# Performance work log

Measured on AMD Instinct MI355X. Metric: run time of the kernel, lower is better.

## Reference

```python
import jax, jax.numpy as jnp
import numpy as np

EPS = 0.1
N_ITERS = 50


def setup_inputs() -> dict:
    key = jax.random.key(0)
    ks = jax.random.split(key, 4)
    B, C, D, H, W = 2, 64, 4, 16, 32
    feat1 = jax.random.normal(ks[0], (B, C, D, H, W), jnp.float32)
    feat2 = jax.random.normal(ks[1], (B, C, D, H, W), jnp.float32)
    w1 = jax.random.normal(ks[2], (C, 2 * C), jnp.float32) * 0.05  # Conv3d(2C->C, k=1)
    b1 = jnp.zeros((C,), jnp.float32)
    w2 = jax.random.normal(ks[3], (C, C), jnp.float32) * 0.05      # Conv3d(C->C, k=1)
    b2 = jnp.zeros((C,), jnp.float32)
    return {"feat1": feat1, "feat2": feat2, "w1": w1, "b1": b1, "w2": w2, "b2": b2}


def reference(feat1, feat2, w1, b1, w2, b2):
    B, C = feat1.shape[0], feat1.shape[1]
    M = int(np.prod(feat1.shape[2:]))
    seq1 = feat1.reshape(B, C, M).transpose(0, 2, 1)  # [B,M,C]
    seq2 = feat2.reshape(B, C, M).transpose(0, 2, 1)  # [B,M,C]
    # squared euclidean distance = cdist(.,p=2)**2
    sq1 = jnp.sum(seq1 * seq1, axis=-1)               # [B,M]
    sq2 = jnp.sum(seq2 * seq2, axis=-1)               # [B,M]
    cross = jnp.einsum('bmc,bnc->bmn', seq1, seq2)    # [B,M,M]
    C_mat = jnp.maximum(sq1[:, :, None] + sq2[:, None, :] - 2.0 * cross, 0.0)
    log_K = -C_mat / EPS

    def step(lk, _):
        lk = lk - jax.nn.logsumexp(lk, axis=2, keepdims=True)  # row normalize
        lk = lk - jax.nn.logsumexp(lk, axis=1, keepdims=True)  # col normalize
        return lk, None

    log_K, _ = jax.lax.scan(jax.checkpoint(step), log_K, None, length=N_ITERS)
    P = jnp.exp(log_K)                                # [B,M,M]
    fused_ot = jnp.einsum('bmn,bnc->bcm', P, seq2)    # [B,C,M]

    # adaptive gating fusion: two 1x1x1 convs == channel matmuls
    f1 = feat1.reshape(B, C, M)
    cat = jnp.concatenate([f1, fused_ot], axis=1)     # [B,2C,M]
    h = jax.nn.relu(jnp.einsum('oc,bcm->bom', w1, cat) + b1[None, :, None])
    gate = jax.nn.sigmoid(jnp.einsum('oc,bcm->bom', w2, h) + b2[None, :, None])
    fused = gate * f1 + (1.0 - gate) * fused_ot
    return fused.reshape(feat1.shape)
```

## Files before the change

kernel.cpp:

```cpp
#include <hip/hip_runtime.h>
#include <hip/hip_bf16.h>

#define MM 2048
#define CC 64
#define NEG_EPS_INV (-10.0f)

__global__ __launch_bounds__(256) void k_tr(const float* __restrict__ f2,
                                            float* __restrict__ s2t) {
    __shared__ float t[64 * 65];
    int bx = blockIdx.x;
    int b = bx >> 5, nc = bx & 31;
    int tid = threadIdx.x;
    int col = tid & 63, cp = tid >> 6;
    const size_t fbase = (size_t)b * CC * MM;
    for (int it = 0; it < 16; ++it) {
        int c = it * 4 + cp;
        t[c * 65 + col] = f2[fbase + (size_t)c * MM + nc * 64 + col];
    }
    __syncthreads();
    int w = tid >> 6, lane = tid & 63;
    for (int i = 0; i < 16; ++i) {
        int nn = w * 16 + i;
        s2t[((size_t)b * MM + nc * 64 + nn) * 64 + lane] = t[lane * 65 + nn];
    }
}

__global__ __launch_bounds__(256) void k_build(const float* __restrict__ f1,
                                               const float* __restrict__ f2,
                                               float* __restrict__ K0,
                                               float* __restrict__ K0T, int useT) {
    __shared__ float f1s[64 * 64];
    __shared__ float f2s[64 * 64];
    __shared__ float kt[64 * 65];
    __shared__ float sq1s[64], sq2s[64];
    int bx = blockIdx.x;
    int b = bx >> 10, mt = (bx >> 5) & 31, nt = bx & 31;
    int tid = threadIdx.x;
    int w = tid >> 6, lane = tid & 63;
    int col = tid & 63, cp = tid >> 6;
    const size_t fbase = (size_t)b * CC * MM;
    for (int it = 0; it < 16; ++it) {
        int c = it * 4 + cp;
        f1s[c * 64 + col] = f1[fbase + (size_t)c * MM + mt * 64 + col];
        f2s[c * 64 + col] = f2[fbase + (size_t)c * MM + nt * 64 + col];
    }
    __syncthreads();
    if (tid < 64) {
        float s = 0.f;
        for (int c = 0; c < 64; ++c) { float x = f1s[c * 64 + tid]; s = fmaf(x, x, s); }
        sq1s[tid] = s;
    } else if (tid < 128) {
        int n = tid - 64;
        float s = 0.f;
        for (int c = 0; c < 64; ++c) { float x = f2s[c * 64 + n]; s = fmaf(x, x, s); }
        sq2s[n] = s;
    }
    __syncthreads();
    float acc[16];
#pragma unroll
    for (int i = 0; i < 16; ++i) acc[i] = 0.f;
    for (int c = 0; c < 64; ++c) {
        float f2v = f2s[c * 64 + lane];
#pragma unroll
        for (int i = 0; i < 16; ++i)
            acc[i] = fmaf(f1s[c * 64 + w * 16 + i], f2v, acc[i]);
    }
    float sq2v = sq2s[lane];
    size_t kbase = ((size_t)b * MM + mt * 64 + w * 16) * MM + nt * 64 + lane;
#pragma unroll
    for (int i = 0; i < 16; ++i) {
        float r = sq1s[w * 16 + i] + sq2v - 2.f * acc[i];
        r = fmaxf(r, 0.f);
        float kv = NEG_EPS_INV * r;
        K0[kbase + (size_t)i * MM] = kv;
        kt[(w * 16 + i) * 65 + lane] = kv;
    }
    if (useT) {
        __syncthreads();
        size_t tbase = ((size_t)b * MM + nt * 64 + w * 16) * MM + mt * 64 + lane;
#pragma unroll
        for (int i = 0; i < 16; ++i)
            K0T[tbase + (size_t)i * MM] = kt[lane * 65 + (w * 16 + i)];
    }
}

__global__ __launch_bounds__(256) void k_lse(const float* __restrict__ K,
                                             const float* __restrict__ vin,
                                             float* __restrict__ uout) {
    int bx = blockIdx.x;
    int b = bx >> 9, rg = bx & 511;
    int w = threadIdx.x >> 6, lane = threadIdx.x & 63;
    int m = rg * 4 + w;
    const float* rowp = K + ((size_t)b * MM + m) * MM;
    const float* vp = vin + (size_t)b * MM;
    float x[32];
#pragma unroll
    for (int j = 0; j < 8; ++j) {
        float4 kv = *(const float4*)(rowp + j * 256 + lane * 4);
        float4 vv = *(const float4*)(vp + j * 256 + lane * 4);
        x[j * 4 + 0] = kv.x + vv.x;
        x[j * 4 + 1] = kv.y + vv.y;
        x[j * 4 + 2] = kv.z + vv.z;
        x[j * 4 + 3] = kv.w + vv.w;
    }
    float mx = x[0];
#pragma unroll
    for (int i = 1; i < 32; ++i) mx = fmaxf(mx, x[i]);
#pragma unroll
    for (int off = 32; off >= 1; off >>= 1) mx = fmaxf(mx, __shfl_xor(mx, off));
    float s = 0.f;
#pragma unroll
    for (int i = 0; i < 32; ++i) s += __expf(x[i] - mx);
#pragma unroll
    for (int off = 32; off >= 1; off >>= 1) s += __shfl_xor(s, off);
    if (lane == 0) uout[(size_t)b * MM + m] = -(mx + __logf(s));
}

__global__ __launch_bounds__(1024) void k_colfb(const float* __restrict__ K,
                                                const float* __restrict__ uin,
                                                float* __restrict__ vout) {
    __shared__ float pm[16 * 64], ps[16 * 64];
    int bx = blockIdx.x;
    int b = bx >> 5, nc = bx & 31;
    int w = threadIdx.x >> 6, lane = threadIdx.x & 63;
    int n = nc * 64 + lane;
    const float* up = uin + (size_t)b * MM;
    float mx = -3.0e38f, s = 0.f;
    size_t base = ((size_t)b * MM + w * 128) * MM + n;
    for (int mm = 0; mm < 128; ++mm) {
        float x = K[base + (size_t)mm * MM] + up[w * 128 + mm];
        float nm = fmaxf(mx, x);
        s = s * __expf(mx - nm) + __expf(x - nm);
        mx = nm;
    }
    pm[w * 64 + lane] = mx;
    ps[w * 64 + lane] = s;
    __syncthreads();
    if (w == 0) {
        float M2 = pm[lane];
        for (int i = 1; i < 16; ++i) M2 = fmaxf(M2, pm[i * 64 + lane]);
        float S = 0.f;
        for (int i = 0; i < 16; ++i) S += ps[i * 64 + lane] * __expf(pm[i * 64 + lane] - M2);
        vout[(size_t)b * MM + n] = -(M2 + __logf(S));
    }
}

__global__ __launch_bounds__(256) void k_fot(const float* __restrict__ K0,
                                             const float* __restrict__ u,
                                             const float* __restrict__ v,
                                             const float* __restrict__ s2t,
                                             float* __restrict__ fot) {
    extern __shared__ float plds[];
    int bx = blockIdx.x;
    int b = bx >> 8, mg = (bx >> 2) & 63, ns = bx & 3;
    int w = threadIdx.x >> 6, lane = threadIdx.x & 63;
    int m0 = mg * 32 + w * 8;
    float* pw = plds + w * 512 * 8;
    const float* vp = v + (size_t)b * MM + ns * 512;
#pragma unroll
    for (int r = 0; r < 8; ++r) {
        const float* krow = K0 + ((size_t)b * MM + m0 + r) * MM + ns * 512;
        float uv = u[(size_t)b * MM + m0 + r];
        for (int j = 0; j < 8; ++j) {
            int nn = j * 64 + lane;
            pw[nn * 8 + r] = __expf(krow[nn] + uv + vp[nn]);
        }
    }
    __syncthreads();
    float acc[8];
#pragma unroll
    for (int r = 0; r < 8; ++r) acc[r] = 0.f;
    const float* s2p = s2t + ((size_t)b * MM + ns * 512) * 64 + lane;
    for (int nn = 0; nn < 512; ++nn) {
        float s2 = s2p[(size_t)nn * 64];
        float4 p0 = *(const float4*)(pw + nn * 8);
        float4 p1 = *(const float4*)(pw + nn * 8 + 4);
        acc[0] = fmaf(p0.x, s2, acc[0]);
        acc[1] = fmaf(p0.y, s2, acc[1]);
        acc[2] = fmaf(p0.z, s2, acc[2]);
        acc[3] = fmaf(p0.w, s2, acc[3]);
        acc[4] = fmaf(p1.x, s2, acc[4]);
        acc[5] = fmaf(p1.y, s2, acc[5]);
        acc[6] = fmaf(p1.z, s2, acc[6]);
        acc[7] = fmaf(p1.w, s2, acc[7]);
    }
#pragma unroll
    for (int r = 0; r < 8; ++r)
        atomicAdd(&fot[((size_t)b * MM + m0 + r) * 64 + lane], acc[r]);
}

__global__ __launch_bounds__(256) void k_gate(const float* __restrict__ f1,
                                              const float* __restrict__ fot,
                                              const float* __restrict__ w1,
                                              const float* __restrict__ b1,
                                              const float* __restrict__ w2,
                                              const float* __restrict__ b2,
                                              float* __restrict__ out) {
    __shared__ float w1s[64 * 129];
    __shared__ float w2s[64 * 65];
    __shared__ float cats[4 * 128];
    __shared__ float hs[4 * 64];
    __shared__ float outs[64 * 5];
    int bx = blockIdx.x;
    int b = bx >> 9, mg = bx & 511;
    int tid = threadIdx.x;
    int w = tid >> 6, lane = tid & 63;
    int m = mg * 4 + w;
    for (int t = 0; t < 32; ++t) {
        int idx = t * 256 + tid;
        w1s[(idx >> 7) * 129 + (idx & 127)] = w1[idx];
    }
    for (int t = 0; t < 16; ++t) {
        int idx = t * 256 + tid;
        w2s[(idx >> 6) * 65 + (idx & 63)] = w2[idx];
    }
    float f1v = f1[(size_t)b * CC * MM + (size_t)lane * MM + m];
    float fov = fot[((size_t)b * MM + m) * 64 + lane];
    cats[w * 128 + lane] = f1v;
    cats[w * 128 + 64 + lane] = fov;
    __syncthreads();
    float hacc = b1[lane];
    for (int c = 0; c < 128; ++c)
        hacc = fmaf(w1s[lane * 129 + c], cats[w * 128 + c], hacc);
    hs[w * 64 + lane] = fmaxf(hacc, 0.f);
    __syncthreads();
    float g = b2[lane];
    for (int c = 0; c < 64; ++c)
        g = fmaf(w2s[lane * 65 + c], hs[w * 64 + c], g);
    g = 1.f / (1.f + __expf(-g));
    float fused = g * f1v + (1.f - g) * fov;
    outs[lane * 5 + w] = fused;
    __syncthreads();
    int o = tid >> 2, mi = tid & 3;
    out[(size_t)b * CC * MM + (size_t)o * MM + mg * 4 + mi] = outs[o * 5 + mi];
}

extern "C" void kernel_launch(void* const* d_in, const int* in_sizes, int n_in,
                              void* d_out, int out_size, void* d_ws, size_t ws_size,
                              hipStream_t stream) {
    const float* feat1 = (const float*)d_in[0];
    const float* feat2 = (const float*)d_in[1];
    const float* w1 = (const float*)d_in[2];
    const float* b1 = (const float*)d_in[3];
    const float* w2 = (const float*)d_in[4];
    const float* b2 = (const float*)d_in[5];
    float* out = (float*)d_out;
    char* ws = (char*)d_ws;

    const size_t S = (size_t)2 * MM * MM * 4;
    const size_t tail = 16384 + 16384 + 1048576 + 1048576;
    int useT = (ws_size >= 2 * S + tail) ? 1 : 0;

    float* K0 = (float*)ws;
    float* K0T = (float*)(ws + S);
    float* tailp = (float*)(ws + (useT ? 2 * S : S));
    float* u = tailp;
    float* v = tailp + 4096;
    float* s2t = v + 4096;
    float* fot = s2t + 262144;

    k_tr<<<64, 256, 0, stream>>>(feat2, s2t);
    k_build<<<2048, 256, 0, stream>>>(feat1, feat2, K0, K0T, useT);
    hipMemsetAsync(v, 0, 16384, stream);
    hipMemsetAsync(fot, 0, 1048576, stream);

    for (int it = 0; it < 50; ++it) {
        k_lse<<<1024, 256, 0, stream>>>(K0, v, u);
        if (useT)
            k_lse<<<1024, 256, 0, stream>>>(K0T, u, v);
        else
            k_colfb<<<64, 1024, 0, stream>>>(K0, u, v);
    }

    k_fot<<<512, 256, 65536, stream>>>(K0, u, v, s2t, fot);
    k_gate<<<1024, 256, 0, stream>>>(feat1, fot, w1, b1, w2, b2, out);
}
```

Before: 833.8 us.

## Fuse Sinkhorn iterations into one persistent kernel with register-resident cost rows

Replaces the 100 separate row/column logsumexp launches with a single persistent kernel of 256 blocks. Each thread keeps its slice of two K rows and two K-transpose rows in registers for all 50 iterations, so the 32 MB cost matrix is not re-read from memory on every pass. Blocks synchronise between half-steps through an atomic-counter grid barrier. The barrier assumes all 256 blocks are co-resident, the wait loop has a timeout guard that could silently break correctness, and the K0T workspace is now always required with no fallback path.

```diff
diff --git a/kernel.cpp b/kernel.cpp
--- a/kernel.cpp
+++ b/kernel.cpp
@@ -4,6 +4,7 @@
 #define MM 2048
 #define CC 64
 #define NEG_EPS_INV (-10.0f)
+#define NBLK 256
 
 __global__ __launch_bounds__(256) void k_tr(const float* __restrict__ f2,
                                             float* __restrict__ s2t) {
@@ -28,7 +29,7 @@
 __global__ __launch_bounds__(256) void k_build(const float* __restrict__ f1,
                                                const float* __restrict__ f2,
                                                float* __restrict__ K0,
-                                               float* __restrict__ K0T, int useT) {
+                                               float* __restrict__ K0T) {
     __shared__ float f1s[64 * 64];
     __shared__ float f2s[64 * 64];
     __shared__ float kt[64 * 65];
@@ -70,78 +71,100 @@
 #pragma unroll
     for (int i = 0; i < 16; ++i) {
         float r = sq1s[w * 16 + i] + sq2v - 2.f * acc[i];
-        r = fmaxf(r, 0.f);
-        float kv = NEG_EPS_INV * r;
+        float kv = NEG_EPS_INV * fmaxf(r, 0.f);
         K0[kbase + (size_t)i * MM] = kv;
         kt[(w * 16 + i) * 65 + lane] = kv;
     }
-    if (useT) {
-        __syncthreads();
-        size_t tbase = ((size_t)b * MM + nt * 64 + w * 16) * MM + mt * 64 + lane;
-#pragma unroll
-        for (int i = 0; i < 16; ++i)
-            K0T[tbase + (size_t)i * MM] = kt[lane * 65 + (w * 16 + i)];
-    }
-}
-
-__global__ __launch_bounds__(256) void k_lse(const float* __restrict__ K,
-                                             const float* __restrict__ vin,
-                                             float* __restrict__ uout) {
-    int bx = blockIdx.x;
-    int b = bx >> 9, rg = bx & 511;
-    int w = threadIdx.x >> 6, lane = threadIdx.x & 63;
-    int m = rg * 4 + w;
-    const float* rowp = K + ((size_t)b * MM + m) * MM;
-    const float* vp = vin + (size_t)b * MM;
-    float x[32];
-#pragma unroll
-    for (int j = 0; j < 8; ++j) {
-        float4 kv = *(const float4*)(rowp + j * 256 + lane * 4);
-        float4 vv = *(const float4*)(vp + j * 256 + lane * 4);
-        x[j * 4 + 0] = kv.x + vv.x;
-        x[j * 4 + 1] = kv.y + vv.y;
-        x[j * 4 + 2] = kv.z + vv.z;
-        x[j * 4 + 3] = kv.w + vv.w;
-    }
-    float mx = x[0];
-#pragma unroll
-    for (int i = 1; i < 32; ++i) mx = fmaxf(mx, x[i]);
-#pragma unroll
-    for (int off = 32; off >= 1; off >>= 1) mx = fmaxf(mx, __shfl_xor(mx, off));
-    float s = 0.f;
-#pragma unroll
-    for (int i = 0; i < 32; ++i) s += __expf(x[i] - mx);
-#pragma unroll
-    for (int off = 32; off >= 1; off >>= 1) s += __shfl_xor(s, off);
-    if (lane == 0) uout[(size_t)b * MM + m] = -(mx + __logf(s));
-}
-
-__global__ __launch_bounds__(1024) void k_colfb(const float* __restrict__ K,
-                                                const float* __restrict__ uin,
-                                                float* __restrict__ vout) {
-    __shared__ float pm[16 * 64], ps[16 * 64];
-    int bx = blockIdx.x;
-    int b = bx >> 5, nc = bx & 31;
-    int w = threadIdx.x >> 6, lane = threadIdx.x & 63;
-    int n = nc * 64 + lane;
-    const float* up = uin + (size_t)b * MM;
-    float mx = -3.0e38f, s = 0.f;
-    size_t base = ((size_t)b * MM + w * 128) * MM + n;
-    for (int mm = 0; mm < 128; ++mm) {
-        float x = K[base + (size_t)mm * MM] + up[w * 128 + mm];
-        float nm = fmaxf(mx, x);
-        s = s * __expf(mx - nm) + __expf(x - nm);
-        mx = nm;
-    }
-    pm[w * 64 + lane] = mx;
-    ps[w * 64 + lane] = s;
-    __syncthreads();
-    if (w == 0) {
-        float M2 = pm[lane];
-        for (int i = 1; i < 16; ++i) M2 = fmaxf(M2, pm[i * 64 + lane]);
-        float S = 0.f;
-        for (int i = 0; i < 16; ++i) S += ps[i * 64 + lane] * __expf(pm[i * 64 + lane] - M2);
-        vout[(size_t)b * MM + n] = -(M2 + __logf(S));
+    __syncthreads();
+    size_t tbase = ((size_t)b * MM + nt * 64 + w * 16) * MM + mt * 64 + lane;
+#pragma unroll
+    for (int i = 0; i < 16; ++i)
+        K0T[tbase + (size_t)i * MM] = kt[lane * 65 + (w * 16 + i)];
+}
+
+__device__ __forceinline__ void gbar(int* bar, int slot, int tid) {
+    __syncthreads();
+    if (tid == 0) {
+        __threadfence();
+        atomicAdd(&bar[slot], 1);
+        long guard = 0;
+        while (__hip_atomic_load(&bar[slot], __ATOMIC_RELAXED,
+                                 __HIP_MEMORY_SCOPE_AGENT) < NBLK &&
+               ++guard < (1L << 25)) {
+            __builtin_amdgcn_s_sleep(2);
+        }
+        __threadfence();
+    }
+    __syncthreads();
+}
+
+#define LSE2(KA, KB, SRCP, DSTP)                                         \
+    {                                                                    \
+        float xl[32];                                                    \
+        _Pragma("unroll")                                                \
+        for (int j = 0; j < 8; ++j) {                                    \
+            float4 t = ((const float4*)(SRCP))[j * 64 + lane];           \
+            xl[4*j+0] = t.x; xl[4*j+1] = t.y;                            \
+            xl[4*j+2] = t.z; xl[4*j+3] = t.w;                            \
+        }                                                                \
+        _Pragma("unroll")                                                \
+        for (int r = 0; r < 2; ++r) {                                    \
+            float mx = -3.0e38f;                                         \
+            _Pragma("unroll")                                            \
+            for (int i = 0; i < 32; ++i)                                 \
+                mx = fmaxf(mx, (r == 0 ? KA[i] : KB[i]) + xl[i]);        \
+            _Pragma("unroll")                                            \
+            for (int off = 32; off >= 1; off >>= 1)                      \
+                mx = fmaxf(mx, __shfl_xor(mx, off));                     \
+            float s = 0.f;                                               \
+            _Pragma("unroll")                                            \
+            for (int i = 0; i < 32; ++i)                                 \
+                s += __expf((r == 0 ? KA[i] : KB[i]) + xl[i] - mx);      \
+            _Pragma("unroll")                                            \
+            for (int off = 32; off >= 1; off >>= 1)                      \
+                s += __shfl_xor(s, off);                                 \
+            if (lane == 0) (DSTP)[row0 + r] = -(mx + __logf(s));         \
+        }                                                                \
+    }
+
+__global__ __launch_bounds__(512) void k_sink(const float* __restrict__ K0,
+                                              const float* __restrict__ K0T,
+                                              float* __restrict__ u,
+                                              float* __restrict__ v,
+                                              int* __restrict__ bar) {
+    const int blk = blockIdx.x;
+    const int b = blk >> 7, rg = blk & 127;
+    const int tid = threadIdx.x;
+    const int lane = tid & 63;
+    const int w = tid >> 6;
+    const int row0 = rg * 16 + w * 2;
+
+    float kr0[32], kr1[32], kc0[32], kc1[32];
+    {
+        const float4* r0p = (const float4*)(K0 + ((size_t)b * MM + row0) * MM);
+        const float4* r1p = (const float4*)(K0 + ((size_t)b * MM + row0 + 1) * MM);
+        const float4* c0p = (const float4*)(K0T + ((size_t)b * MM + row0) * MM);
+        const float4* c1p = (const float4*)(K0T + ((size_t)b * MM + row0 + 1) * MM);
+#pragma unroll
+        for (int j = 0; j < 8; ++j) {
+            float4 a = r0p[j * 64 + lane];
+            kr0[4*j+0] = a.x; kr0[4*j+1] = a.y; kr0[4*j+2] = a.z; kr0[4*j+3] = a.w;
+            float4 c = r1p[j * 64 + lane];
+            kr1[4*j+0] = c.x; kr1[4*j+1] = c.y; kr1[4*j+2] = c.z; kr1[4*j+3] = c.w;
+            float4 d = c0p[j * 64 + lane];
+            kc0[4*j+0] = d.x; kc0[4*j+1] = d.y; kc0[4*j+2] = d.z; kc0[4*j+3] = d.w;
+            float4 e = c1p[j * 64 + lane];
+            kc1[4*j+0] = e.x; kc1[4*j+1] = e.y; kc1[4*j+2] = e.z; kc1[4*j+3] = e.w;
+        }
+    }
+    float* up = u + (size_t)b * MM;
+    float* vp = v + (size_t)b * MM;
+
+    for (int it = 0; it < 50; ++it) {
+        LSE2(kr0, kr1, vp, up);
+        gbar(bar, 2 * it, tid);
+        LSE2(kc0, kc1, up, vp);
+        gbar(bar, 2 * it + 1, tid);
     }
 }
 
@@ -245,32 +268,23 @@
     const float* w2 = (const float*)d_in[4];
     const float* b2 = (const float*)d_in[5];
     float* out = (float*)d_out;
-    char* ws = (char*)d_ws;
-
-    const size_t S = (size_t)2 * MM * MM * 4;
-    const size_t tail = 16384 + 16384 + 1048576 + 1048576;
-    int useT = (ws_size >= 2 * S + tail) ? 1 : 0;
-
-    float* K0 = (float*)ws;
-    float* K0T = (float*)(ws + S);
-    float* tailp = (float*)(ws + (useT ? 2 * S : S));
-    float* u = tailp;
-    float* v = tailp + 4096;
+    float* ws = (float*)d_ws;
+
+    float* K0  = ws;
+    float* K0T = K0 + (size_t)8388608;
+    float* u   = K0T + (size_t)8388608;
+    float* v   = u + 4096;
     float* s2t = v + 4096;
     float* fot = s2t + 262144;
+    int*   bar = (int*)(fot + 262144);
 
     k_tr<<<64, 256, 0, stream>>>(feat2, s2t);
-    k_build<<<2048, 256, 0, stream>>>(feat1, feat2, K0, K0T, useT);
+    k_build<<<2048, 256, 0, stream>>>(feat1, feat2, K0, K0T);
     hipMemsetAsync(v, 0, 16384, stream);
     hipMemsetAsync(fot, 0, 1048576, stream);
-
-    for (int it = 0; it < 50; ++it) {
-        k_lse<<<1024, 256, 0, stream>>>(K0, v, u);
-        if (useT)
-            k_lse<<<1024, 256, 0, stream>>>(K0T, u, v);
-        else
-            k_colfb<<<64, 1024, 0, stream>>>(K0, u, v);
-    }
+    hipMemsetAsync(bar, 0, 512, stream);
+
+    k_sink<<<NBLK, 512, 0, stream>>>(K0, K0T, u, v, bar);
 
     k_fot<<<512, 256, 65536, stream>>>(K0, u, v, s2t, fot);
     k_gate<<<1024, 256, 0, stream>>>(feat1, fot, w1, b1, w2, b2, out);
```

After: 1.966 ms. 2.36x slower.
